# Kernel tuning notes

Hardware: AMD Instinct MI355X
Metric: run time of the kernel (lower is better)

The kernel has to match this reference:

```python
import jax, jax.numpy as jnp
import numpy as np

B, N = 4, 1024
DIM, DEPTH, HEADS, DHEAD, MLP = 512, 6, 8, 64, 2048
INNER = HEADS * DHEAD
SCALE = DHEAD ** -0.5
EPS = 1e-5


def setup_inputs() -> dict:
    key = jax.random.key(0)
    ks = jax.random.split(key, 16)
    w = lambda k, shape: (jax.random.normal(k, shape, jnp.float32) * 0.02)
    D = DEPTH
    return {
        "g": jax.random.normal(ks[0], (B, N, DIM), jnp.float32),
        "x": jax.random.normal(ks[1], (B, N, DIM), jnp.float32),
        # PreNorm + SelfAttention
        "ln1_s": jnp.ones((D, DIM)), "ln1_b": jnp.zeros((D, DIM)),
        "Wqkv": w(ks[2], (D, DIM, 3 * INNER)),
        "Wo_sa": w(ks[3], (D, INNER, DIM)), "bo_sa": jnp.zeros((D, DIM)),
        # RelationalCrossAttention
        "lng_s": jnp.ones((D, DIM)), "lng_b": jnp.zeros((D, DIM)),
        "lnx_s": jnp.ones((D, DIM)), "lnx_b": jnp.zeros((D, DIM)),
        "Wq": w(ks[4], (D, DIM, INNER)),
        "Wk": w(ks[5], (D, DIM, INNER)),
        "Wv": w(ks[6], (D, DIM, INNER)), "bv": jnp.zeros((D, INNER)),
        "Wo_ca": w(ks[7], (D, INNER, DIM)), "bo_ca": jnp.zeros((D, DIM)),
        # PreNorm + FeedForward (same module applied twice per layer)
        "lnf_s": jnp.ones((D, DIM)), "lnf_b": jnp.zeros((D, DIM)),
        "W1": w(ks[8], (D, DIM, MLP)), "b1": jnp.zeros((D, MLP)),
        "W2": w(ks[9], (D, MLP, DIM)), "b2": jnp.zeros((D, DIM)),
    }


def _ln(t, s, b):
    m = t.mean(-1, keepdims=True)
    v = ((t - m) ** 2).mean(-1, keepdims=True)
    return (t - m) / jnp.sqrt(v + EPS) * s + b


def _split_heads(t):  # [b, n, h*d] -> [b, h, n, d]
    b, n, _ = t.shape
    return t.reshape(b, n, HEADS, DHEAD).transpose(0, 2, 1, 3)


def _merge_heads(t):  # [b, h, n, d] -> [b, n, h*d]
    b, h, n, d = t.shape
    return t.transpose(0, 2, 1, 3).reshape(b, n, h * d)


def _attend(q, k, v):
    dots = jnp.einsum('bhnd,bhmd->bhnm', q, k) * SCALE
    attn = jax.nn.softmax(jnp.nan_to_num(dots, nan=-jnp.inf), axis=-1)
    attn = jnp.nan_to_num(attn)  # nan_to_num(0.0) post-softmax as in source
    return jnp.einsum('bhnm,bhmd->bhnd', attn, jnp.nan_to_num(v))


def reference(g, x, ln1_s, ln1_b, Wqkv, Wo_sa, bo_sa, lng_s, lng_b, lnx_s, lnx_b,
              Wq, Wk, Wv, bv, Wo_ca, bo_ca, lnf_s, lnf_b, W1, b1, W2, b2):
    for i in range(DEPTH):
        def ff(t):
            h = jax.nn.gelu(_ln(t, lnf_s[i], lnf_b[i]) @ W1[i] + b1[i], approximate=False)
            return h @ W2[i] + b2[i]
        # relational cross attention: q,k from g, v from x
        gn = _ln(g, lng_s[i], lng_b[i])
        xn = _ln(x, lnx_s[i], lnx_b[i])
        q = _split_heads(gn @ Wq[i])
        k = _split_heads(gn @ Wk[i])
        v = _split_heads(xn @ Wv[i] + bv[i])
        x = _merge_heads(_attend(q, k, v)) @ Wo_ca[i] + bo_ca[i] + x
        x = ff(x) + x
        # pre-norm self attention (skip connection enabled)
        sn = _ln(x, ln1_s[i], ln1_b[i])
        qkv = sn @ Wqkv[i]
        qs, ks_, vs = jnp.split(qkv, 3, axis=-1)
        sa = _merge_heads(_attend(_split_heads(qs), _split_heads(ks_), _split_heads(vs)))
        x = sa @ Wo_sa[i] + bo_sa[i] + x
        x = ff(x) + x
    return x
```

## Files before the change

### kernel.cpp

```cpp
#include <hip/hip_runtime.h>
#include <hip/hip_bf16.h>
#include <cstdint>
#include <cstddef>

#define DEV __device__ __forceinline__

using f32x4 = __attribute__((ext_vector_type(4))) float;
using bfx8  = __attribute__((ext_vector_type(8))) __bf16;
using s16x8 = __attribute__((ext_vector_type(8))) short;

DEV uint16_t f2bf(float f) {
    union { float f; uint32_t u; } x; x.f = f;
    uint32_t r = x.u + 0x7fffu + ((x.u >> 16) & 1u);
    return (uint16_t)(r >> 16);
}

DEV float gelu_exact(float v) {
    return 0.5f * v * (1.0f + erff(v * 0.70710678118654752f));
}

DEV f32x4 mfma16(s16x8 a, s16x8 b, f32x4 c) {
    return __builtin_amdgcn_mfma_f32_16x16x32_bf16(
        __builtin_bit_cast(bfx8, a), __builtin_bit_cast(bfx8, b), c, 0, 0, 0);
}

DEV void async_lds16(const void* g, void* l) {
    __builtin_amdgcn_global_load_lds(
        (const __attribute__((address_space(1))) uint32_t*)g,
        (__attribute__((address_space(3))) uint32_t*)l, 16, 0, 0);
}

template<int N> DEV void wait_vmcnt() {
    if constexpr (N == 0)      asm volatile("s_waitcnt vmcnt(0)" ::: "memory");
    else if constexpr (N == 4) asm volatile("s_waitcnt vmcnt(4)" ::: "memory");
    else if constexpr (N == 8) asm volatile("s_waitcnt vmcnt(8)" ::: "memory");
    else static_assert(N == 0 || N == 4 || N == 8, "add vmcnt literal");
}
#define SBAR      asm volatile("s_barrier" ::: "memory")
#define LGKM0     asm volatile("s_waitcnt lgkmcnt(0)" ::: "memory")
#define SCHED0    __builtin_amdgcn_sched_barrier(0)

DEV void ln_row(const float* __restrict__ in, const float* __restrict__ sc,
                const float* __restrict__ bi, uint16_t* __restrict__ out, size_t row)
{
    const int lane = threadIdx.x & 63;
    const float* p = in + row * 512 + lane * 8;
    float4 a = *(const float4*)p;
    float4 b4 = *(const float4*)(p + 4);
    float v[8] = {a.x, a.y, a.z, a.w, b4.x, b4.y, b4.z, b4.w};
    float s = 0.f, sq = 0.f;
#pragma unroll
    for (int j = 0; j < 8; ++j) { s += v[j]; sq += v[j] * v[j]; }
#pragma unroll
    for (int o = 1; o < 64; o <<= 1) { s += __shfl_xor(s, o); sq += __shfl_xor(sq, o); }
    const float mean = s * (1.0f / 512.0f);
    const float var  = sq * (1.0f / 512.0f) - mean * mean;
    const float rstd = rsqrtf(var + 1e-5f);
    const int c = lane * 8;
    uint16_t o8[8];
#pragma unroll
    for (int j = 0; j < 8; ++j)
        o8[j] = f2bf((v[j] - mean) * rstd * sc[c + j] + bi[c + j]);
    uint4 pk;
    pk.x = (uint32_t)o8[0] | ((uint32_t)o8[1] << 16);
    pk.y = (uint32_t)o8[2] | ((uint32_t)o8[3] << 16);
    pk.z = (uint32_t)o8[4] | ((uint32_t)o8[5] << 16);
    pk.w = (uint32_t)o8[6] | ((uint32_t)o8[7] << 16);
    *reinterpret_cast<uint4*>(out + row * 512 + c) = pk;
}

__global__ __launch_bounds__(256)
void ln_bf16(const float* __restrict__ in, const float* __restrict__ sc,
             const float* __restrict__ bi, uint16_t* __restrict__ out)
{
    ln_row(in, sc, bi, out, (size_t)blockIdx.x * 4 + (threadIdx.x >> 6));
}

__global__ __launch_bounds__(256)
void ln2_bf16(const float* __restrict__ in0, const float* __restrict__ sc0,
              const float* __restrict__ bi0, uint16_t* __restrict__ out0,
              const float* __restrict__ in1, const float* __restrict__ sc1,
              const float* __restrict__ bi1, uint16_t* __restrict__ out1)
{
    const int sel = blockIdx.x >> 10;
    const size_t row = (size_t)(blockIdx.x & 1023) * 4 + (threadIdx.x >> 6);
    if (sel == 0) ln_row(in0, sc0, bi0, out0, row);
    else          ln_row(in1, sc1, bi1, out1, row);
}

__global__ __launch_bounds__(256)
void wtrans(const float* __restrict__ W, uint16_t* __restrict__ WT, int K, int N,
            size_t lstride, int row0)
{
    __shared__ float tile[32][33];
    const int l = blockIdx.z;
    const int k0 = blockIdx.x * 32, n0 = blockIdx.y * 32;
    const float* Wl = W + (size_t)l * K * N;
    uint16_t* WTl = WT + (size_t)l * lstride;
    const int tx = threadIdx.x, ty = threadIdx.y;
#pragma unroll
    for (int j = 0; j < 4; ++j)
        tile[ty + j * 8][tx] = Wl[(size_t)(k0 + ty + j * 8) * N + n0 + tx];
    __syncthreads();
#pragma unroll
    for (int j = 0; j < 4; ++j)
        WTl[(size_t)(row0 + n0 + ty + j * 8) * K + k0 + tx] = f2bf(tile[tx][ty + j * 8]);
}

__global__ __launch_bounds__(256)
void vtrans(const uint16_t* __restrict__ src, uint16_t* __restrict__ vt, int C, int coff)
{
    __shared__ uint16_t tile[64][72];
    const int n0 = blockIdx.x * 64;
    const int bh = blockIdx.y, b = bh >> 3, h = bh & 7;
    const int tx = threadIdx.x, ty = threadIdx.y;
#pragma unroll
    for (int j = 0; j < 16; ++j) {
        const int n = ty + j * 4;
        tile[n][tx] = src[((size_t)b * 1024 + n0 + n) * C + coff + h * 64 + tx];
    }
    __syncthreads();
    uint16_t* o = vt + (size_t)bh * 65536;
#pragma unroll
    for (int j = 0; j < 16; ++j) {
        const int d = ty + j * 4;
        o[(size_t)d * 1024 + n0 + tx] = tile[tx][d];
    }
}

template<int BM, int BN, int NWR, int NWC, int MINW,
         int HAS_BIAS, int HAS_RESID, int DO_GELU, int OUT_BF16>
__global__ __launch_bounds__(256, MINW)
void gemm4(const uint16_t* __restrict__ A, const uint16_t* __restrict__ BT,
           const float* __restrict__ bias, const float* __restrict__ resid,
           void* __restrict__ outp, int M, int N, int K)
{
    constexpr int WM = BM / NWR, WN = BN / NWC;
    constexpr int FM = WM / 16, FN = WN / 16;
    constexpr int ASLOTS = 8 * BM, BSLOTS = 8 * BN, TOT = ASLOTS + BSLOTS;
    constexpr int S = TOT / 256;
    __shared__ uint16_t As[2][ASLOTS * 8];
    __shared__ uint16_t Bs[2][BSLOTS * 8];
    const int tid = threadIdx.x, lane = tid & 63;
    const int w = tid >> 6, wr = w / NWC, wc = w % NWC;
    const int kg = lane >> 4, lr = lane & 15;
    const int nwg = gridDim.x;
    const int id0 = blockIdx.x;
    const int id = (id0 & 7) * (nwg >> 3) + (id0 >> 3);
    const int nbn = N / BN;
    const size_t m0 = (size_t)(id / nbn) * BM;
    const size_t n0 = (size_t)(id % nbn) * BN;

    auto stage = [&](int b, int k0) {
#pragma unroll
        for (int j = 0; j < S; ++j) {
            const int s = j * 256 + tid;
            if (s < ASLOTS) {
                const int sub = s / BM, row = s % BM;
                async_lds16(A + (m0 + row) * K + k0 + sub * 8, &As[b][s * 8]);
            } else {
                const int s2 = s - ASLOTS;
                const int sub = s2 / BN, row = s2 % BN;
                async_lds16(BT + (n0 + row) * K + k0 + sub * 8, &Bs[b][s2 * 8]);
            }
        }
    };

    f32x4 acc[FM][FN] = {};
    const int nt = K / 64;
    stage(0, 0);
    stage(1, 64);
    int cur = 0;
    for (int t = 0; t < nt; ++t) {
        if (t < nt - 1) wait_vmcnt<S>(); else wait_vmcnt<0>();
        SBAR;
        s16x8 af[2][FM], bf[2][FN];
#pragma unroll
        for (int ks = 0; ks < 2; ++ks) {
#pragma unroll
            for (int i = 0; i < FM; ++i)
                af[ks][i] = *(const s16x8*)&As[cur][((ks * 4 + kg) * BM + wr * WM + i * 16 + lr) * 8];
#pragma unroll
            for (int j = 0; j < FN; ++j)
                bf[ks][j] = *(const s16x8*)&Bs[cur][((ks * 4 + kg) * BN + wc * WN + j * 16 + lr) * 8];
        }
        __builtin_amdgcn_s_setprio(1);
#pragma unroll
        for (int ks = 0; ks < 2; ++ks)
#pragma unroll
            for (int i = 0; i < FM; ++i)
#pragma unroll
                for (int j = 0; j < FN; ++j)
                    acc[i][j] = mfma16(af[ks][i], bf[ks][j], acc[i][j]);
        __builtin_amdgcn_s_setprio(0);
        LGKM0; SCHED0;
        SBAR;
        if (t + 2 < nt) stage(cur, (t + 2) * 64);
        cur ^= 1;
    }
#pragma unroll
    for (int i = 0; i < FM; ++i) {
        const size_t rbase = m0 + wr * WM + i * 16 + kg * 4;
#pragma unroll
        for (int j = 0; j < FN; ++j) {
            const size_t col = n0 + wc * WN + j * 16 + lr;
            const float bval = HAS_BIAS ? bias[col] : 0.0f;
#pragma unroll
            for (int r = 0; r < 4; ++r) {
                const size_t row = rbase + r;
                float v = acc[i][j][r] + bval;
                if (DO_GELU)  v = gelu_exact(v);
                if (HAS_RESID) v += resid[row * (size_t)N + col];
                if (OUT_BF16) ((uint16_t*)outp)[row * (size_t)N + col] = f2bf(v);
                else          ((float*)outp)[row * (size_t)N + col] = v;
            }
        }
    }
}

__global__ __launch_bounds__(256)
void attn_flash(const uint16_t* __restrict__ Qb, const uint16_t* __restrict__ Kb,
                const uint16_t* __restrict__ Vt, uint16_t* __restrict__ Ob,
                int qstride, int kstride, int qoff, int koff)
{
    __shared__ uint16_t Ks[2][4096];
    __shared__ uint16_t Vs[2][4096];
    __shared__ uint16_t Pb[4][1024];
    const int tid = threadIdx.x, lane = tid & 63, w = tid >> 6;
    const int kg = lane >> 4, lr = lane & 15;
    const int bh = blockIdx.y, b = bh >> 3, h = bh & 7;
    const int q0 = blockIdx.x * 64;
    const float CEXP = 0.125f * 1.44269504f;

    s16x8 aq0, aq1;
    {
        const size_t qrow = (size_t)b * 1024 + q0 + w * 16 + lr;
        const uint16_t* qp = Qb + qrow * qstride + qoff + h * 64 + kg * 8;
        aq0 = *(const s16x8*)qp;
        aq1 = *(const s16x8*)(qp + 32);
    }
    const uint16_t* kbase = Kb + (size_t)b * 1024 * kstride + koff + h * 64;
    const uint16_t* vbase = Vt + (size_t)bh * 65536;

    float l_r[4] = {0.f, 0.f, 0.f, 0.f};
    f32x4 acc[4] = {};

    auto stage = [&](int buf, int kv0) {
#pragma unroll
        for (int j = 0; j < 2; ++j) {
            const int s = j * 256 + tid;
            const int sub = s >> 6, row = s & 63;
            async_lds16(kbase + (size_t)(kv0 + row) * kstride + sub * 8, &Ks[buf][s * 8]);
            async_lds16(vbase + (size_t)row * 1024 + kv0 + sub * 8,      &Vs[buf][s * 8]);
        }
    };

    stage(0, 0);
    __syncthreads();
    int cur = 0;
    for (int t = 0; t < 16; ++t) {
        if (t < 15) stage(cur ^ 1, (t + 1) * 64);
        f32x4 s4[4];
        __builtin_amdgcn_s_setprio(1);
#pragma unroll
        for (int ni = 0; ni < 4; ++ni) {
            s16x8 bk0 = *(const s16x8*)&Ks[cur][(kg * 64 + ni * 16 + lr) * 8];
            s16x8 bk1 = *(const s16x8*)&Ks[cur][((4 + kg) * 64 + ni * 16 + lr) * 8];
            f32x4 z = {};
            z = mfma16(aq0, bk0, z);
            z = mfma16(aq1, bk1, z);
            s4[ni] = z;
        }
        __builtin_amdgcn_s_setprio(0);
#pragma unroll
        for (int ni = 0; ni < 4; ++ni) {
            const int slotb = (ni * 2 + (lr >> 3)) * 16 + kg * 4;
#pragma unroll
            for (int r = 0; r < 4; ++r) {
                const float pe = __builtin_amdgcn_exp2f(s4[ni][r] * CEXP);
                l_r[r] += pe;
                Pb[w][(slotb + r) * 8 + (lr & 7)] = f2bf(pe);
            }
        }
        s16x8 ap0 = *(const s16x8*)&Pb[w][(kg * 16 + lr) * 8];
        s16x8 ap1 = *(const s16x8*)&Pb[w][((4 + kg) * 16 + lr) * 8];
        __builtin_amdgcn_s_setprio(1);
#pragma unroll
        for (int ni = 0; ni < 4; ++ni) {
            s16x8 bv0 = *(const s16x8*)&Vs[cur][(kg * 64 + ni * 16 + lr) * 8];
            s16x8 bv1 = *(const s16x8*)&Vs[cur][((4 + kg) * 64 + ni * 16 + lr) * 8];
            acc[ni] = mfma16(ap0, bv0, acc[ni]);
            acc[ni] = mfma16(ap1, bv1, acc[ni]);
        }
        __builtin_amdgcn_s_setprio(0);
        __syncthreads();
        cur ^= 1;
    }
    float linv[4];
#pragma unroll
    for (int r = 0; r < 4; ++r) {
        float l = l_r[r];
        l += __shfl_xor(l, 1); l += __shfl_xor(l, 2);
        l += __shfl_xor(l, 4); l += __shfl_xor(l, 8);
        linv[r] = 1.0f / l;
    }
#pragma unroll
    for (int ni = 0; ni < 4; ++ni)
#pragma unroll
        for (int r = 0; r < 4; ++r) {
            const float v = acc[ni][r] * linv[r];
            const size_t row = (size_t)b * 1024 + q0 + w * 16 + kg * 4 + r;
            Ob[row * 512 + h * 64 + ni * 16 + lr] = f2bf(v);
        }
}

extern "C" void kernel_launch(void* const* d_in, const int* in_sizes, int n_in,
                              void* d_out, int out_size, void* d_ws, size_t ws_size,
                              hipStream_t stream)
{
    (void)in_sizes; (void)n_in; (void)out_size; (void)ws_size;
    const float* g     = (const float*)d_in[0];
    const float* x0    = (const float*)d_in[1];
    const float* ln1_s = (const float*)d_in[2];
    const float* ln1_b = (const float*)d_in[3];
    const float* Wqkv  = (const float*)d_in[4];
    const float* Wo_sa = (const float*)d_in[5];
    const float* bo_sa = (const float*)d_in[6];
    const float* lng_s = (const float*)d_in[7];
    const float* lng_b = (const float*)d_in[8];
    const float* lnx_s = (const float*)d_in[9];
    const float* lnx_b = (const float*)d_in[10];
    const float* Wq    = (const float*)d_in[11];
    const float* Wk    = (const float*)d_in[12];
    const float* Wv    = (const float*)d_in[13];
    const float* bv    = (const float*)d_in[14];
    const float* Wo_ca = (const float*)d_in[15];
    const float* bo_ca = (const float*)d_in[16];
    const float* lnf_s = (const float*)d_in[17];
    const float* lnf_b = (const float*)d_in[18];
    const float* W1    = (const float*)d_in[19];
    const float* b1    = (const float*)d_in[20];
    const float* W2    = (const float*)d_in[21];
    const float* b2    = (const float*)d_in[22];

    float* x = (float*)d_out;

    char* p = (char*)d_ws;
    auto carve = [&](size_t n) { char* r = p; p += (n + 255) & ~(size_t)255; return r; };
    uint16_t* WqkT  = (uint16_t*)carve(6ull * 1024 * 512 * 2);
    uint16_t* WvT   = (uint16_t*)carve(6ull * 512 * 512 * 2);
    uint16_t* WocaT = (uint16_t*)carve(6ull * 512 * 512 * 2);
    uint16_t* WqkvT = (uint16_t*)carve(6ull * 1536 * 512 * 2);
    uint16_t* WosaT = (uint16_t*)carve(6ull * 512 * 512 * 2);
    uint16_t* W1T   = (uint16_t*)carve(6ull * 2048 * 512 * 2);
    uint16_t* W2T   = (uint16_t*)carve(6ull * 512 * 2048 * 2);
    uint16_t* gn    = (uint16_t*)carve(4096ull * 512 * 2);
    uint16_t* xn    = (uint16_t*)carve(4096ull * 512 * 2);
    uint16_t* qkvu  = (uint16_t*)carve(4096ull * 1536 * 2);
    uint16_t* vt    = (uint16_t*)carve(32ull * 64 * 1024 * 2);
    uint16_t* ab    = (uint16_t*)carve(4096ull * 512 * 2);
    uint16_t* hb    = (uint16_t*)carve(4096ull * 2048 * 2);
    uint16_t* qk = qkvu;
    uint16_t* vb = qkvu + 4096ull * 1024;

    dim3 tb(32, 8);
    wtrans<<<dim3(16, 16, 6), tb, 0, stream>>>(Wq,    WqkT,  512, 512,  1024ull * 512, 0);
    wtrans<<<dim3(16, 16, 6), tb, 0, stream>>>(Wk,    WqkT,  512, 512,  1024ull * 512, 512);
    wtrans<<<dim3(16, 16, 6), tb, 0, stream>>>(Wv,    WvT,   512, 512,  512ull * 512, 0);
    wtrans<<<dim3(16, 16, 6), tb, 0, stream>>>(Wo_ca, WocaT, 512, 512,  512ull * 512, 0);
    wtrans<<<dim3(16, 48, 6), tb, 0, stream>>>(Wqkv,  WqkvT, 512, 1536, 1536ull * 512, 0);
    wtrans<<<dim3(16, 16, 6), tb, 0, stream>>>(Wo_sa, WosaT, 512, 512,  512ull * 512, 0);
    wtrans<<<dim3(16, 64, 6), tb, 0, stream>>>(W1,    W1T,   512, 2048, 2048ull * 512, 0);
    wtrans<<<dim3(64, 16, 6), tb, 0, stream>>>(W2,    W2T,   2048, 512, 2048ull * 512, 0);

    hipMemcpyAsync(x, x0, 4096ull * 512 * 4, hipMemcpyDeviceToDevice, stream);

    const dim3 ga(16, 32), va(16, 32), vb4(64, 4);

    for (int l = 0; l < 6; ++l) {
        const size_t o512 = (size_t)l * 512, oW = (size_t)l * 512 * 512;
        const size_t oW1 = (size_t)l * 2048 * 512, oWqkv = (size_t)l * 1536 * 512;
        const size_t o2048 = (size_t)l * 2048;

        ln2_bf16<<<2048, 256, 0, stream>>>(g, lng_s + o512, lng_b + o512, gn,
                                           x, lnx_s + o512, lnx_b + o512, xn);
        gemm4<64, 64, 2, 2, 4, 0, 0, 0, 1><<<1024, 256, 0, stream>>>(
            gn, WqkT + (size_t)l * 1024 * 512, nullptr, nullptr, qk, 4096, 1024, 512);
        gemm4<64, 64, 2, 2, 4, 1, 0, 0, 1><<<512, 256, 0, stream>>>(
            xn, WvT + oW, bv + o512, nullptr, vb, 4096, 512, 512);
        vtrans<<<va, vb4, 0, stream>>>(vb, vt, 512, 0);
        attn_flash<<<ga, 256, 0, stream>>>(qk, qk, vt, ab, 1024, 1024, 0, 512);
        gemm4<64, 64, 2, 2, 4, 1, 1, 0, 0><<<512, 256, 0, stream>>>(
            ab, WocaT + oW, bo_ca + o512, x, x, 4096, 512, 512);

        ln_bf16<<<1024, 256, 0, stream>>>(x, lnf_s + o512, lnf_b + o512, xn);
        gemm4<128, 128, 2, 2, 2, 1, 0, 1, 1><<<512, 256, 0, stream>>>(
            xn, W1T + oW1, b1 + o2048, nullptr, hb, 4096, 2048, 512);
        gemm4<64, 64, 2, 2, 4, 1, 1, 0, 0><<<512, 256, 0, stream>>>(
            hb, W2T + oW1, b2 + o512, x, x, 4096, 512, 2048);

        ln_bf16<<<1024, 256, 0, stream>>>(x, ln1_s + o512, ln1_b + o512, xn);
        gemm4<64, 64, 2, 2, 4, 0, 0, 0, 1><<<1536, 256, 0, stream>>>(
            xn, WqkvT + oWqkv, nullptr, nullptr, qkvu, 4096, 1536, 512);
        vtrans<<<va, vb4, 0, stream>>>(qkvu, vt, 1536, 1024);
        attn_flash<<<ga, 256, 0, stream>>>(qkvu, qkvu, vt, ab, 1536, 1536, 0, 512);
        gemm4<64, 64, 2, 2, 4, 1, 1, 0, 0><<<512, 256, 0, stream>>>(
            ab, WosaT + oW, bo_sa + o512, x, x, 4096, 512, 512);

        ln_bf16<<<1024, 256, 0, stream>>>(x, lnf_s + o512, lnf_b + o512, xn);
        gemm4<128, 128, 2, 2, 2, 1, 0, 1, 1><<<512, 256, 0, stream>>>(
            xn, W1T + oW1, b1 + o2048, nullptr, hb, 4096, 2048, 512);
        gemm4<64, 64, 2, 2, 4, 1, 1, 0, 0><<<512, 256, 0, stream>>>(
            hb, W2T + oW1, b2 + o512, x, x, 4096, 512, 2048);
    }
}
```

Before: 1.701 ms.

## Split-K the FFN down-projection and retune GEMM tile shapes per layer

The W2 GEMM (K=2048) is split into two K halves that write fp32 partials to a workspace, and a new reduce kernel sums them with the bias and residual. This doubles the block count of a grid that was only 512 blocks. The QK and QKV projections move to 128x128 tiles with 512-thread blocks, and W1 moves to 64x64 tiles with 2048 blocks. The split adds an extra pass over fp32 partials plus one more launch per FFN in exchange for better occupancy.

```diff
diff --git a/kernel.cpp b/kernel.cpp
--- a/kernel.cpp
+++ b/kernel.cpp
@@ -33,8 +33,7 @@
 template<int N> DEV void wait_vmcnt() {
     if constexpr (N == 0)      asm volatile("s_waitcnt vmcnt(0)" ::: "memory");
     else if constexpr (N == 4) asm volatile("s_waitcnt vmcnt(4)" ::: "memory");
-    else if constexpr (N == 8) asm volatile("s_waitcnt vmcnt(8)" ::: "memory");
-    else static_assert(N == 0 || N == 4 || N == 8, "add vmcnt literal");
+    else static_assert(N == 0 || N == 4, "add vmcnt literal");
 }
 #define SBAR      asm volatile("s_barrier" ::: "memory")
 #define LGKM0     asm volatile("s_waitcnt lgkmcnt(0)" ::: "memory")
@@ -129,16 +128,18 @@
 }
 
 template<int BM, int BN, int NWR, int NWC, int MINW,
-         int HAS_BIAS, int HAS_RESID, int DO_GELU, int OUT_BF16>
-__global__ __launch_bounds__(256, MINW)
-void gemm4(const uint16_t* __restrict__ A, const uint16_t* __restrict__ BT,
+         int HAS_BIAS, int HAS_RESID, int DO_GELU, int OUT_BF16, int PARTIAL>
+__global__ __launch_bounds__(NWR * NWC * 64, MINW)
+void gemm5(const uint16_t* __restrict__ A, const uint16_t* __restrict__ BT,
            const float* __restrict__ bias, const float* __restrict__ resid,
-           void* __restrict__ outp, int M, int N, int K)
-{
+           void* __restrict__ outp, int M, int N, int K, int kh)
+{
+    constexpr int NT = NWR * NWC * 64;
     constexpr int WM = BM / NWR, WN = BN / NWC;
     constexpr int FM = WM / 16, FN = WN / 16;
     constexpr int ASLOTS = 8 * BM, BSLOTS = 8 * BN, TOT = ASLOTS + BSLOTS;
-    constexpr int S = TOT / 256;
+    constexpr int S = TOT / NT;
+    static_assert(S == 4, "vmcnt literal assumes S==4");
     __shared__ uint16_t As[2][ASLOTS * 8];
     __shared__ uint16_t Bs[2][BSLOTS * 8];
     const int tid = threadIdx.x, lane = tid & 63;
@@ -150,11 +151,12 @@
     const int nbn = N / BN;
     const size_t m0 = (size_t)(id / nbn) * BM;
     const size_t n0 = (size_t)(id % nbn) * BN;
+    const int kbase = PARTIAL ? blockIdx.y * kh : 0;
 
     auto stage = [&](int b, int k0) {
 #pragma unroll
         for (int j = 0; j < S; ++j) {
-            const int s = j * 256 + tid;
+            const int s = j * NT + tid;
             if (s < ASLOTS) {
                 const int sub = s / BM, row = s % BM;
                 async_lds16(A + (m0 + row) * K + k0 + sub * 8, &As[b][s * 8]);
@@ -167,9 +169,9 @@
     };
 
     f32x4 acc[FM][FN] = {};
-    const int nt = K / 64;
-    stage(0, 0);
-    stage(1, 64);
+    const int nt = kh / 64;
+    stage(0, kbase);
+    stage(1, kbase + 64);
     int cur = 0;
     for (int t = 0; t < nt; ++t) {
         if (t < nt - 1) wait_vmcnt<S>(); else wait_vmcnt<0>();
@@ -195,9 +197,10 @@
         __builtin_amdgcn_s_setprio(0);
         LGKM0; SCHED0;
         SBAR;
-        if (t + 2 < nt) stage(cur, (t + 2) * 64);
+        if (t + 2 < nt) stage(cur, kbase + (t + 2) * 64);
         cur ^= 1;
     }
+    float* pout = PARTIAL ? (float*)outp + (size_t)blockIdx.y * M * (size_t)N : nullptr;
 #pragma unroll
     for (int i = 0; i < FM; ++i) {
         const size_t rbase = m0 + wr * WM + i * 16 + kg * 4;
@@ -209,6 +212,7 @@
             for (int r = 0; r < 4; ++r) {
                 const size_t row = rbase + r;
                 float v = acc[i][j][r] + bval;
+                if (PARTIAL) { pout[row * (size_t)N + col] = v; continue; }
                 if (DO_GELU)  v = gelu_exact(v);
                 if (HAS_RESID) v += resid[row * (size_t)N + col];
                 if (OUT_BF16) ((uint16_t*)outp)[row * (size_t)N + col] = f2bf(v);
@@ -216,6 +220,26 @@
             }
         }
     }
+}
+
+__global__ __launch_bounds__(256)
+void reduce2(const float* __restrict__ p, const float* __restrict__ bias,
+             float* __restrict__ x)
+{
+    const size_t i = ((size_t)blockIdx.x * 256 + threadIdx.x) * 8;
+    const int col = (int)(i & 511);
+    const float* q = p + 4096ull * 512;
+    float4 a0 = *(const float4*)(p + i),     a1 = *(const float4*)(p + i + 4);
+    float4 b0 = *(const float4*)(q + i),     b1 = *(const float4*)(q + i + 4);
+    float4 s0 = *(const float4*)(bias + col), s1 = *(const float4*)(bias + col + 4);
+    float4 r0 = *(const float4*)(x + i),     r1 = *(const float4*)(x + i + 4);
+    float4 o0, o1;
+    o0.x = a0.x + b0.x + s0.x + r0.x;  o0.y = a0.y + b0.y + s0.y + r0.y;
+    o0.z = a0.z + b0.z + s0.z + r0.z;  o0.w = a0.w + b0.w + s0.w + r0.w;
+    o1.x = a1.x + b1.x + s1.x + r1.x;  o1.y = a1.y + b1.y + s1.y + r1.y;
+    o1.z = a1.z + b1.z + s1.z + r1.z;  o1.w = a1.w + b1.w + s1.w + r1.w;
+    *(float4*)(x + i) = o0;
+    *(float4*)(x + i + 4) = o1;
 }
 
 __global__ __launch_bounds__(256)
@@ -360,6 +384,7 @@
     uint16_t* vt    = (uint16_t*)carve(32ull * 64 * 1024 * 2);
     uint16_t* ab    = (uint16_t*)carve(4096ull * 512 * 2);
     uint16_t* hb    = (uint16_t*)carve(4096ull * 2048 * 2);
+    float*    pk2   = (float*)carve(2ull * 4096 * 512 * 4);
     uint16_t* qk = qkvu;
     uint16_t* vb = qkvu + 4096ull * 1024;
 
@@ -384,33 +409,35 @@
 
         ln2_bf16<<<2048, 256, 0, stream>>>(g, lng_s + o512, lng_b + o512, gn,
                                            x, lnx_s + o512, lnx_b + o512, xn);
-        gemm4<64, 64, 2, 2, 4, 0, 0, 0, 1><<<1024, 256, 0, stream>>>(
-            gn, WqkT + (size_t)l * 1024 * 512, nullptr, nullptr, qk, 4096, 1024, 512);
-        gemm4<64, 64, 2, 2, 4, 1, 0, 0, 1><<<512, 256, 0, stream>>>(
-            xn, WvT + oW, bv + o512, nullptr, vb, 4096, 512, 512);
+        gemm5<128, 128, 2, 4, 4, 0, 0, 0, 1, 0><<<256, 512, 0, stream>>>(
+            gn, WqkT + (size_t)l * 1024 * 512, nullptr, nullptr, qk, 4096, 1024, 512, 512);
+        gemm5<64, 64, 2, 2, 4, 1, 0, 0, 1, 0><<<512, 256, 0, stream>>>(
+            xn, WvT + oW, bv + o512, nullptr, vb, 4096, 512, 512, 512);
         vtrans<<<va, vb4, 0, stream>>>(vb, vt, 512, 0);
         attn_flash<<<ga, 256, 0, stream>>>(qk, qk, vt, ab, 1024, 1024, 0, 512);
-        gemm4<64, 64, 2, 2, 4, 1, 1, 0, 0><<<512, 256, 0, stream>>>(
-            ab, WocaT + oW, bo_ca + o512, x, x, 4096, 512, 512);
+        gemm5<64, 64, 2, 2, 4, 1, 1, 0, 0, 0><<<512, 256, 0, stream>>>(
+            ab, WocaT + oW, bo_ca + o512, x, x, 4096, 512, 512, 512);
 
         ln_bf16<<<1024, 256, 0, stream>>>(x, lnf_s + o512, lnf_b + o512, xn);
-        gemm4<128, 128, 2, 2, 2, 1, 0, 1, 1><<<512, 256, 0, stream>>>(
-            xn, W1T + oW1, b1 + o2048, nullptr, hb, 4096, 2048, 512);
-        gemm4<64, 64, 2, 2, 4, 1, 1, 0, 0><<<512, 256, 0, stream>>>(
-            hb, W2T + oW1, b2 + o512, x, x, 4096, 512, 2048);
+        gemm5<64, 64, 2, 2, 4, 1, 0, 1, 1, 0><<<2048, 256, 0, stream>>>(
+            xn, W1T + oW1, b1 + o2048, nullptr, hb, 4096, 2048, 512, 512);
+        gemm5<64, 64, 2, 2, 4, 0, 0, 0, 0, 1><<<dim3(512, 2), 256, 0, stream>>>(
+            hb, W2T + oW1, nullptr, nullptr, pk2, 4096, 512, 2048, 1024);
+        reduce2<<<1024, 256, 0, stream>>>(pk2, b2 + o512, x);
 
         ln_bf16<<<1024, 256, 0, stream>>>(x, ln1_s + o512, ln1_b + o512, xn);
-        gemm4<64, 64, 2, 2, 4, 0, 0, 0, 1><<<1536, 256, 0, stream>>>(
-            xn, WqkvT + oWqkv, nullptr, nullptr, qkvu, 4096, 1536, 512);
+        gemm5<128, 128, 2, 4, 4, 0, 0, 0, 1, 0><<<384, 512, 0, stream>>>(
+            xn, WqkvT + oWqkv, nullptr, nullptr, qkvu, 4096, 1536, 512, 512);
         vtrans<<<va, vb4, 0, stream>>>(qkvu, vt, 1536, 1024);
         attn_flash<<<ga, 256, 0, stream>>>(qkvu, qkvu, vt, ab, 1536, 1536, 0, 512);
-        gemm4<64, 64, 2, 2, 4, 1, 1, 0, 0><<<512, 256, 0, stream>>>(
-            ab, WosaT + oW, bo_sa + o512, x, x, 4096, 512, 512);
+        gemm5<64, 64, 2, 2, 4, 1, 1, 0, 0, 0><<<512, 256, 0, stream>>>(
+            ab, WosaT + oW, bo_sa + o512, x, x, 4096, 512, 512, 512);
 
         ln_bf16<<<1024, 256, 0, stream>>>(x, lnf_s + o512, lnf_b + o512, xn);
-        gemm4<128, 128, 2, 2, 2, 1, 0, 1, 1><<<512, 256, 0, stream>>>(
-            xn, W1T + oW1, b1 + o2048, nullptr, hb, 4096, 2048, 512);
-        gemm4<64, 64, 2, 2, 4, 1, 1, 0, 0><<<512, 256, 0, stream>>>(
-            hb, W2T + oW1, b2 + o512, x, x, 4096, 512, 2048);
-    }
-}
+        gemm5<64, 64, 2, 2, 4, 1, 0, 1, 1, 0><<<2048, 256, 0, stream>>>(
+            xn, W1T + oW1, b1 + o2048, nullptr, hb, 4096, 2048, 512, 512);
+        gemm5<64, 64, 2, 2, 4, 0, 0, 0, 0, 1><<<dim3(512, 2), 256, 0, stream>>>(
+            hb, W2T + oW1, nullptr, nullptr, pk2, 4096, 512, 2048, 1024);
+        reduce2<<<1024, 256, 0, stream>>>(pk2, b2 + o512, x);
+    }
+}
```

Measured after the change: 1.826 ms. +7.3%, slower.
